# Performance work log

Hardware: AMD Instinct MI355X
Metric: run time of the kernel (lower is better)

## Reference

```python
import jax, jax.numpy as jnp
import numpy as np

NGH, POS_D, NEG_D, SUB_D, BORDER = 7, 3, 5, 1, 16

def _offsets():
    rad = NGH // SUB_D * NGH
    pos, neg = [], []
    for j in range(-rad, rad + 1, SUB_D):
        for i in range(-rad, rad + 1, SUB_D):
            d2 = i * i + j * j
            if d2 <= POS_D ** 2:
                pos.append((i, j))
            elif NEG_D ** 2 <= d2 <= NGH ** 2:
                neg.append((i, j))
    return (jnp.asarray(np.array(pos, np.int32).T),  # [2, P] rows (dy, dx)
            jnp.asarray(np.array(neg, np.int32).T))  # [2, Ng]

POS_OFF, NEG_OFF = _offsets()

def bilinear(pos, feat):
    # pos [N,2]=(y,x) float coords in feature-map scale; feat [C,h,w] -> [N,C]
    C, h, w = feat.shape
    y = jnp.clip(pos[:, 0], 0.0, h - 1.0)
    x = jnp.clip(pos[:, 1], 0.0, w - 1.0)
    y0 = jnp.floor(y); x0 = jnp.floor(x)
    y0i = y0.astype(jnp.int32); x0i = x0.astype(jnp.int32)
    y1i = jnp.minimum(y0i + 1, h - 1); x1i = jnp.minimum(x0i + 1, w - 1)
    wy = (y - y0)[:, None]; wx = (x - x0)[:, None]
    g = lambda yi, xi: feat[:, yi, xi].T  # [N,C]
    return ((1 - wy) * (1 - wx) * g(y0i, x0i) + (1 - wy) * wx * g(y0i, x1i)
            + wy * (1 - wx) * g(y1i, x0i) + wy * wx * g(y1i, x1i))

def l2norm(x):
    return x / jnp.maximum(jnp.linalg.norm(x, axis=-1, keepdims=True), 1e-12)

def clamp_yx(p, H, W):
    return jnp.stack([jnp.clip(p[..., 0], 0.0, H - 1.0),
                      jnp.clip(p[..., 1], 0.0, W - 1.0)], axis=-1)

def _per_image(f0, f1, c0, c1, p0, p1, H, W, N):
    # all points are generated inside the border, so the border mask keeps all;
    # rnd_sample -> deterministic first-N / last-N subsample
    vp0 = p0[:N].astype(jnp.float32)          # [N,2]
    vp1 = p1[:N].astype(jnp.float32)
    vf0 = l2norm(bilinear(vp0 / 4, f0))       # [N,128]
    qconf = bilinear(vp0 / 4, c0)[:, 0]       # [N]
    mask = ((vp1[:, 1] >= 0) & (vp1[:, 1] < W) & (vp1[:, 0] >= 0) & (vp1[:, 0] < H))
    def cand_scores(off):
        P = off.shape[1]
        cand = clamp_yx(vp1[None, :, :] + off.T[:, None, :].astype(jnp.float32), H, W)  # [P,N,2]
        fc = l2norm(bilinear(cand.reshape(-1, 2) / 4, f1).reshape(P, N, -1))
        return jnp.einsum('nc,pnc->np', vf0, fc)  # [N,P]
    ps = cand_scores(POS_OFF)
    pidx = jnp.argmax(ps, axis=1)
    pscore = jnp.max(ps, axis=1, keepdims=True)   # [N,1] (maxpool over pos ngh)
    sel = clamp_yx(vp1 + POS_OFF.T[pidx].astype(jnp.float32), H, W)
    qconf = (qconf + bilinear(sel / 4, c1)[:, 0]) / 2
    nscores = cand_scores(NEG_OFF)                # [N,Ng]
    vp2 = p1[p1.shape[0] - N:].astype(jnp.float32)  # independent subsample for distractors
    dist = l2norm(bilinear(vp2 / 4, f1))          # [N,128]
    return pscore, nscores, dist, vf0, vp1, vp2, qconf, mask

def reference(feat0, feat1, conf0, conf1, pos0, pos1, B, H, W, N):
    fn = jax.vmap(lambda a, b, c, d, e, f: _per_image(a, b, c, d, e, f, H, W, N))
    pscore, ns, dist, vf0, vp1, vp2, qconf, mask = fn(feat0, feat1, conf0, conf1, pos0, pos1)
    BN = B * N
    pscores = pscore.reshape(BN, 1)
    nscores = ns.reshape(BN, -1)
    dist = dist.reshape(BN, -1)
    vf0 = vf0.reshape(BN, -1)
    vp1 = vp1.reshape(BN, 2)
    vp2 = vp2.reshape(BN, 2)
    dscores = vf0 @ dist.T  # [BN,BN]
    dis2 = ((vp2[None, :, 1] - vp1[:, None, 1]) ** 2
            + (vp2[None, :, 0] - vp1[:, None, 0]) ** 2)
    b = jnp.repeat(jnp.arange(BN) // N, 1)
    b = jnp.arange(B).repeat(N)
    dis2 = dis2 + ((b[None, :] != b[:, None]) * (NEG_D ** 2)).astype(dis2.dtype)
    dscores = jnp.where(dis2 < NEG_D ** 2, 0.0, dscores)
    scores = jnp.concatenate([pscores, nscores, dscores], axis=1)
    gt = jnp.zeros(scores.shape, jnp.uint8).at[:, :pscores.shape[1]].set(1)
    return scores, gt, mask, qconf

def setup_inputs() -> dict:
    key = jax.random.key(0)
    ks = jax.random.split(key, 6)
    B, H, W, M, N = 4, 512, 512, 2500, 2000
    h, w, C = H // 4, W // 4, 128
    feat0 = jax.random.normal(ks[0], (B, C, h, w), jnp.float32)
    feat1 = jax.random.normal(ks[1], (B, C, h, w), jnp.float32)
    conf0 = jax.random.uniform(ks[2], (B, 1, h, w), jnp.float32)
    conf1 = jax.random.uniform(ks[3], (B, 1, h, w), jnp.float32)
    pos0 = jax.random.randint(ks[4], (B, M, 2), BORDER, H - BORDER).astype(jnp.int32)
    pos1 = jax.random.randint(ks[5], (B, M, 2), BORDER, H - BORDER).astype(jnp.int32)
    return dict(feat0=feat0, feat1=feat1, conf0=conf0, conf1=conf1,
                pos0=pos0, pos1=pos1, B=B, H=H, W=W, N=N)
```

## Files before the change

kernel.cpp:

```cpp
#include <hip/hip_runtime.h>

typedef unsigned short ushort_t;
typedef __attribute__((ext_vector_type(8))) short bf16x8;
typedef __attribute__((ext_vector_type(4))) float f32x4;

#define BB 4
#define HH 512
#define WW 512
#define NPT 2000
#define MPT 2500
#define CCH 128
#define FH 128
#define FW 128
#define FHW (FH*FW)
#define BNP (BB*NPT)
#define NPOSC 29
#define NNEGC 80
#define NCOL (1 + NNEGC + BNP)

__constant__ int c_pos_dy[NPOSC] = {
  0,
  -2,-1,0,1,2,
  -2,-1,0,1,2,
  -3,-2,-1,0,1,2,3,
  -2,-1,0,1,2,
  -2,-1,0,1,2,
  0};
__constant__ int c_pos_dx[NPOSC] = {
  -3,
  -2,-2,-2,-2,-2,
  -1,-1,-1,-1,-1,
  0,0,0,0,0,0,0,
  1,1,1,1,1,
  2,2,2,2,2,
  3};
__constant__ int c_neg_dy[NNEGC] = {
  0,
  -3,-2,-1,0,1,2,3,
  -4,-3,-2,-1,0,1,2,3,4,
  -5,-4,-3,3,4,5,
  -6,-5,-4,4,5,6,
  -6,-5,5,6,
  -6,-5,5,6,
  -7,-6,-5,5,6,7,
  -6,-5,5,6,
  -6,-5,5,6,
  -6,-5,-4,4,5,6,
  -5,-4,-3,3,4,5,
  -4,-3,-2,-1,0,1,2,3,4,
  -3,-2,-1,0,1,2,3,
  0};
__constant__ int c_neg_dx[NNEGC] = {
  -7,
  -6,-6,-6,-6,-6,-6,-6,
  -5,-5,-5,-5,-5,-5,-5,-5,-5,
  -4,-4,-4,-4,-4,-4,
  -3,-3,-3,-3,-3,-3,
  -2,-2,-2,-2,
  -1,-1,-1,-1,
  0,0,0,0,0,0,
  1,1,1,1,
  2,2,2,2,
  3,3,3,3,3,3,
  4,4,4,4,4,4,
  5,5,5,5,5,5,5,5,5,
  6,6,6,6,6,6,6,
  7};

__device__ __forceinline__ ushort_t f2bf(float f) {
  unsigned u = __float_as_uint(f);
  unsigned r = (u + 0x7fffu + ((u >> 16) & 1u)) >> 16;
  return (ushort_t)r;
}

__device__ __forceinline__ float2 sample2(const float* __restrict__ fb,
                                          float fy, float fx, int lane) {
  float y = fminf(fmaxf(fy, 0.f), (float)(FH - 1));
  float x = fminf(fmaxf(fx, 0.f), (float)(FW - 1));
  float y0 = floorf(y), x0 = floorf(x);
  int iy0 = (int)y0, ix0 = (int)x0;
  int iy1 = min(iy0 + 1, FH - 1), ix1 = min(ix0 + 1, FW - 1);
  float wy = y - y0, wx = x - x0;
  float w00 = (1.f - wy) * (1.f - wx), w01 = (1.f - wy) * wx;
  float w10 = wy * (1.f - wx),         w11 = wy * wx;
  int c = 2 * lane;
  float2 a00 = *(const float2*)(fb + ((size_t)iy0 * FW + ix0) * CCH + c);
  float2 a01 = *(const float2*)(fb + ((size_t)iy0 * FW + ix1) * CCH + c);
  float2 a10 = *(const float2*)(fb + ((size_t)iy1 * FW + ix0) * CCH + c);
  float2 a11 = *(const float2*)(fb + ((size_t)iy1 * FW + ix1) * CCH + c);
  float2 r;
  r.x = w00 * a00.x + w01 * a01.x + w10 * a10.x + w11 * a11.x;
  r.y = w00 * a00.y + w01 * a01.y + w10 * a10.y + w11 * a11.y;
  return r;
}

__device__ __forceinline__ float conf_sample(const float* __restrict__ cb,
                                             float py, float px) {
  float y = fminf(fmaxf(py * 0.25f, 0.f), (float)(FH - 1));
  float x = fminf(fmaxf(px * 0.25f, 0.f), (float)(FW - 1));
  float y0 = floorf(y), x0 = floorf(x);
  int iy0 = (int)y0, ix0 = (int)x0;
  int iy1 = min(iy0 + 1, FH - 1), ix1 = min(ix0 + 1, FW - 1);
  float wy = y - y0, wx = x - x0;
  return (1.f - wy) * (1.f - wx) * cb[iy0 * FW + ix0]
       + (1.f - wy) * wx         * cb[iy0 * FW + ix1]
       + wy * (1.f - wx)         * cb[iy1 * FW + ix0]
       + wy * wx                 * cb[iy1 * FW + ix1];
}

__device__ __forceinline__ float wave_sum(float v) {
#pragma unroll
  for (int o = 32; o > 0; o >>= 1) v += __shfl_xor(v, o, 64);
  return v;
}

__device__ __forceinline__ void cand_partial(const float* __restrict__ fb,
                                             int py, int px, int dy, int dx,
                                             int sub, const float* __restrict__ a8,
                                             float& dot, float& ss) {
  float cy = fminf(fmaxf((float)(py + dy), 0.f), (float)(HH - 1)) * 0.25f;
  float cx = fminf(fmaxf((float)(px + dx), 0.f), (float)(WW - 1)) * 0.25f;
  float y = fminf(cy, (float)(FH - 1));
  float x = fminf(cx, (float)(FW - 1));
  float y0 = floorf(y), x0 = floorf(x);
  int iy0 = (int)y0, ix0 = (int)x0;
  int iy1 = min(iy0 + 1, FH - 1), ix1 = min(ix0 + 1, FW - 1);
  float wy = y - y0, wx = x - x0;
  float w00 = (1.f - wy) * (1.f - wx), w01 = (1.f - wy) * wx;
  float w10 = wy * (1.f - wx),         w11 = wy * wx;
  const float* p00 = fb + ((size_t)iy0 * FW + ix0) * CCH + sub * 8;
  const float* p01 = fb + ((size_t)iy0 * FW + ix1) * CCH + sub * 8;
  const float* p10 = fb + ((size_t)iy1 * FW + ix0) * CCH + sub * 8;
  const float* p11 = fb + ((size_t)iy1 * FW + ix1) * CCH + sub * 8;
  float c00[8], c01[8], c10[8], c11[8];
  *(float4*)&c00[0] = *(const float4*)p00; *(float4*)&c00[4] = *(const float4*)(p00 + 4);
  *(float4*)&c01[0] = *(const float4*)p01; *(float4*)&c01[4] = *(const float4*)(p01 + 4);
  *(float4*)&c10[0] = *(const float4*)p10; *(float4*)&c10[4] = *(const float4*)(p10 + 4);
  *(float4*)&c11[0] = *(const float4*)p11; *(float4*)&c11[4] = *(const float4*)(p11 + 4);
  float d = 0.f, s = 0.f;
#pragma unroll
  for (int ch = 0; ch < 8; ++ch) {
    float v = w00 * c00[ch] + w01 * c01[ch] + w10 * c10[ch] + w11 * c11[ch];
    d += a8[ch] * v;
    s += v * v;
  }
  dot = d; ss = s;
}

__device__ __forceinline__ void better(float& best, int& bidx, float ob, int oi) {
  if (ob > best || (ob == best && oi < bidx)) { best = ob; bidx = oi; }
}

__global__ __launch_bounds__(256) void k_transpose(const float* __restrict__ feat0,
                                                   const float* __restrict__ feat1,
                                                   float* __restrict__ ft0,
                                                   float* __restrict__ ft1) {
  __shared__ float tile[32][33];
  int z = blockIdx.z;
  const float* src = (z < BB) ? feat0 + (size_t)z * CCH * FHW
                              : feat1 + (size_t)(z - BB) * CCH * FHW;
  float* dst = (z < BB) ? ft0 + (size_t)z * CCH * FHW
                        : ft1 + (size_t)(z - BB) * CCH * FHW;
  int p0 = blockIdx.x * 32;
  int c0 = blockIdx.y * 32;
  int tx = threadIdx.x & 31, ty = threadIdx.x >> 5;
#pragma unroll
  for (int jj = 0; jj < 32; jj += 8)
    tile[ty + jj][tx] = src[(size_t)(c0 + ty + jj) * FHW + p0 + tx];
  __syncthreads();
#pragma unroll
  for (int jj = 0; jj < 32; jj += 8)
    dst[(size_t)(p0 + ty + jj) * CCH + c0 + tx] = tile[tx][ty + jj];
}

__global__ __launch_bounds__(256) void k_prep(const float* __restrict__ ft0,
                                              const float* __restrict__ ft1,
                                              const int* __restrict__ pos0,
                                              const int* __restrict__ pos1,
                                              float* __restrict__ vf0,
                                              ushort_t* __restrict__ vf0_bf,
                                              ushort_t* __restrict__ dist_bf,
                                              float* __restrict__ mask_out) {
  int wv = threadIdx.x >> 6, lane = threadIdx.x & 63;
  int n = blockIdx.x * 4 + wv;
  int b = n / NPT, r = n % NPT;

  {
    const float* fb = ft0 + (size_t)b * FHW * CCH;
    float py = (float)pos0[(b * MPT + r) * 2 + 0];
    float px = (float)pos0[(b * MPT + r) * 2 + 1];
    float2 v = sample2(fb, py * 0.25f, px * 0.25f, lane);
    float ss = wave_sum(v.x * v.x + v.y * v.y);
    float inv = 1.f / fmaxf(sqrtf(ss), 1e-12f);
    v.x *= inv; v.y *= inv;
    *(float2*)(vf0 + (size_t)n * CCH + 2 * lane) = v;
    ushort2 p; p.x = f2bf(v.x); p.y = f2bf(v.y);
    *(ushort2*)(vf0_bf + (size_t)n * CCH + 2 * lane) = p;
  }

  {
    const float* fb = ft1 + (size_t)b * FHW * CCH;
    float py = (float)pos1[(b * MPT + (MPT - NPT) + r) * 2 + 0];
    float px = (float)pos1[(b * MPT + (MPT - NPT) + r) * 2 + 1];
    float2 v = sample2(fb, py * 0.25f, px * 0.25f, lane);
    float ss = wave_sum(v.x * v.x + v.y * v.y);
    float inv = 1.f / fmaxf(sqrtf(ss), 1e-12f);
    v.x *= inv; v.y *= inv;
    ushort2 p; p.x = f2bf(v.x); p.y = f2bf(v.y);
    *(ushort2*)(dist_bf + (size_t)n * CCH + 2 * lane) = p;
  }

  if (lane == 0) {
    int my = pos1[(b * MPT + r) * 2 + 0];
    int mx = pos1[(b * MPT + r) * 2 + 1];
    mask_out[n] = (mx >= 0 && mx < WW && my >= 0 && my < HH) ? 1.f : 0.f;
  }
}

__global__ __launch_bounds__(256) void k_zero(float4* __restrict__ p, int n4) {
  int i = blockIdx.x * blockDim.x + threadIdx.x;
  int stride = gridDim.x * blockDim.x;
  float4 z; z.x = 0.f; z.y = 0.f; z.z = 0.f; z.w = 0.f;
  for (; i < n4; i += stride) p[i] = z;
}

__global__ __launch_bounds__(256) void k_cand(const float* __restrict__ ft1,
                                              const float* __restrict__ conf0,
                                              const float* __restrict__ conf1,
                                              const int* __restrict__ pos0,
                                              const int* __restrict__ pos1,
                                              const float* __restrict__ vf0,
                                              float* __restrict__ scores,
                                              float* __restrict__ gt,
                                              float* __restrict__ qconf_out) {
  int n = blockIdx.x;
  int b = n / NPT, r = n % NPT;
  int tid = threadIdx.x;
  int lane = tid & 63, wv = tid >> 6;
  int g = lane >> 4;
  int sub = lane & 15;
  const float* fb1 = ft1 + (size_t)b * FHW * CCH;
  int py = pos1[(b * MPT + r) * 2 + 0];
  int px = pos1[(b * MPT + r) * 2 + 1];

  float a8[8];
  *(float4*)&a8[0] = *(const float4*)(vf0 + (size_t)n * CCH + sub * 8);
  *(float4*)&a8[4] = *(const float4*)(vf0 + (size_t)n * CCH + sub * 8 + 4);

  __shared__ float s_best[4];
  __shared__ int   s_idx[4];

  float best = -1e30f; int bidx = 0x7fffffff;
#pragma unroll
  for (int it = 0; it < 2; ++it) {
    int p = it * 16 + wv * 4 + g;
    int pc = min(p, NPOSC - 1);
    float dot, ss;
    cand_partial(fb1, py, px, c_pos_dy[pc], c_pos_dx[pc], sub, a8, dot, ss);
#pragma unroll
    for (int o = 1; o < 16; o <<= 1) {
      dot += __shfl_xor(dot, o, 64);
      ss  += __shfl_xor(ss,  o, 64);
    }
    float sc = dot / fmaxf(sqrtf(ss), 1e-12f);
    if (p < NPOSC && sc > best) { best = sc; bidx = p; }
  }
  {
    float ob = __shfl_xor(best, 16, 64); int oi = __shfl_xor(bidx, 16, 64);
    better(best, bidx, ob, oi);
    ob = __shfl_xor(best, 32, 64); oi = __shfl_xor(bidx, 32, 64);
    better(best, bidx, ob, oi);
  }
  if (lane == 0) { s_best[wv] = best; s_idx[wv] = bidx; }
  __syncthreads();
  if (tid == 0) {
    float bb = s_best[0]; int bi = s_idx[0];
#pragma unroll
    for (int w2 = 1; w2 < 4; ++w2) better(bb, bi, s_best[w2], s_idx[w2]);
    scores[(size_t)n * NCOL] = bb;
    gt[(size_t)n * NCOL] = 1.0f;
    float q0 = conf_sample(conf0 + (size_t)b * FHW,
                           (float)pos0[(b * MPT + r) * 2 + 0],
                           (float)pos0[(b * MPT + r) * 2 + 1]);
    float sy = fminf(fmaxf((float)(py + c_pos_dy[bi]), 0.f), (float)(HH - 1));
    float sx = fminf(fmaxf((float)(px + c_pos_dx[bi]), 0.f), (float)(WW - 1));
    float q1 = conf_sample(conf1 + (size_t)b * FHW, sy, sx);
    qconf_out[n] = 0.5f * (q0 + q1);
  }

#pragma unroll
  for (int it = 0; it < 5; ++it) {
    int p = it * 16 + wv * 4 + g;
    float dot, ss;
    cand_partial(fb1, py, px, c_neg_dy[p], c_neg_dx[p], sub, a8, dot, ss);
#pragma unroll
    for (int o = 1; o < 16; o <<= 1) {
      dot += __shfl_xor(dot, o, 64);
      ss  += __shfl_xor(ss,  o, 64);
    }
    if (sub == 0)
      scores[(size_t)n * NCOL + 1 + p] = dot / fmaxf(sqrtf(ss), 1e-12f);
  }
}

__global__ __launch_bounds__(256) void k_gemm(const ushort_t* __restrict__ vf0_bf,
                                              const ushort_t* __restrict__ dist_bf,
                                              const int* __restrict__ pos1,
                                              float* __restrict__ scores) {
  int i0 = blockIdx.x * 128, j0 = blockIdx.y * 128;
  int tid = threadIdx.x, lane = tid & 63, wv = tid >> 6;
  int wm = wv >> 1, wn = wv & 1;
  int mrow = lane & 15, quad = lane >> 4;

  __shared__ float s_ry[128], s_rx[128], s_rb[128];
  __shared__ float s_cy[128], s_cx[128], s_cb[128];
  if (tid < 128) {
    int i = min(i0 + tid, BNP - 1);
    int b = i / NPT, rr = i - b * NPT;
    s_ry[tid] = (float)pos1[(b * MPT + rr) * 2 + 0];
    s_rx[tid] = (float)pos1[(b * MPT + rr) * 2 + 1];
    s_rb[tid] = (float)b;
  } else {
    int t2 = tid - 128;
    int j = min(j0 + t2, BNP - 1);
    int b = j / NPT, rr = j - b * NPT;
    s_cy[t2] = (float)pos1[(b * MPT + (MPT - NPT) + rr) * 2 + 0];
    s_cx[t2] = (float)pos1[(b * MPT + (MPT - NPT) + rr) * 2 + 1];
    s_cb[t2] = (float)b;
  }
  __syncthreads();

  f32x4 acc[4][4] = {};
  const ushort_t* abase = vf0_bf  + (size_t)(i0 + wm * 64 + mrow) * CCH + quad * 8;
  const ushort_t* bbase = dist_bf + (size_t)(j0 + wn * 64 + mrow) * CCH + quad * 8;
#pragma unroll
  for (int ks = 0; ks < 4; ++ks) {
    bf16x8 af[4], bf[4];
#pragma unroll
    for (int f = 0; f < 4; ++f) {
      af[f] = *(const bf16x8*)(abase + (size_t)f * 16 * CCH + ks * 32);
      bf[f] = *(const bf16x8*)(bbase + (size_t)f * 16 * CCH + ks * 32);
    }
#pragma unroll
    for (int fm = 0; fm < 4; ++fm)
#pragma unroll
      for (int fn = 0; fn < 4; ++fn)
        acc[fm][fn] = __builtin_amdgcn_mfma_f32_16x16x32_bf16(af[fm], bf[fn],
                                                              acc[fm][fn], 0, 0, 0);
  }

  float cy[4], cx[4], cb[4]; int colg[4];
#pragma unroll
  for (int fn = 0; fn < 4; ++fn) {
    int cl = wn * 64 + fn * 16 + mrow;
    cy[fn] = s_cy[cl]; cx[fn] = s_cx[cl]; cb[fn] = s_cb[cl];
    colg[fn] = j0 + cl;
  }
#pragma unroll
  for (int fm = 0; fm < 4; ++fm) {
#pragma unroll
    for (int reg = 0; reg < 4; ++reg) {
      int rl = wm * 64 + fm * 16 + quad * 4 + reg;
      int row = i0 + rl;
      if (row >= BNP) continue;
      float ry = s_ry[rl], rx = s_rx[rl], rb = s_rb[rl];
      size_t base = (size_t)row * NCOL + 1 + NNEGC;
#pragma unroll
      for (int fn = 0; fn < 4; ++fn) {
        if (colg[fn] >= BNP) continue;
        float dy = cy[fn] - ry, dx = cx[fn] - rx;
        float d2 = dy * dy + dx * dx + ((cb[fn] != rb) ? 25.f : 0.f);
        scores[base + colg[fn]] = (d2 < 25.f) ? 0.f : acc[fm][fn][reg];
      }
    }
  }
}

extern "C" void kernel_launch(void* const* d_in, const int* in_sizes, int n_in,
                              void* d_out, int out_size, void* d_ws, size_t ws_size,
                              hipStream_t stream) {
  (void)in_sizes; (void)n_in; (void)out_size; (void)ws_size;
  const float* feat0 = (const float*)d_in[0];
  const float* feat1 = (const float*)d_in[1];
  const float* conf0 = (const float*)d_in[2];
  const float* conf1 = (const float*)d_in[3];
  const int*   pos0  = (const int*)d_in[4];
  const int*   pos1  = (const int*)d_in[5];

  float* ws = (float*)d_ws;
  float* ft0 = ws;
  float* ft1 = ft0 + (size_t)BB * CCH * FHW;
  float* vf0 = ft1 + (size_t)BB * CCH * FHW;
  ushort_t* vf0_bf  = (ushort_t*)(vf0 + (size_t)BNP * CCH);
  ushort_t* dist_bf = vf0_bf + (size_t)BNP * CCH;

  float* out    = (float*)d_out;
  float* scores = out;
  float* gt     = out + (size_t)BNP * NCOL;
  float* maskp  = gt + (size_t)BNP * NCOL;
  float* qconf  = maskp + BNP;

  dim3 g1(FHW / 32, CCH / 32, 2 * BB);
  k_transpose<<<g1, dim3(256), 0, stream>>>(feat0, feat1, ft0, ft1);
  k_prep<<<dim3(BNP / 4), dim3(256), 0, stream>>>(ft0, ft1, pos0, pos1,
                                                  vf0, vf0_bf, dist_bf, maskp);
  int n4 = (BNP * NCOL) / 4;
  k_zero<<<dim3(8192), dim3(256), 0, stream>>>((float4*)gt, n4);
  k_cand<<<dim3(BNP), dim3(256), 0, stream>>>(ft1, conf0, conf1, pos0, pos1,
                                              vf0, scores, gt, qconf);
  dim3 g5((BNP + 127) / 128, (BNP + 127) / 128);
  k_gemm<<<g5, dim3(256), 0, stream>>>(vf0_bf, dist_bf, pos1, scores);
}
```

Measured before the change: 756.1 us.

## Fuse prep and gt zeroing into candidate kernel, stage feature patch in LDS

```diff
diff --git a/kernel.cpp b/kernel.cpp
--- a/kernel.cpp
+++ b/kernel.cpp
@@ -17,6 +17,7 @@
 #define NPOSC 29
 #define NNEGC 80
 #define NCOL (1 + NNEGC + BNP)
+#define PATCH 6
 
 __constant__ int c_pos_dy[NPOSC] = {
   0,
@@ -114,24 +115,26 @@
   return v;
 }
 
-__device__ __forceinline__ void cand_partial(const float* __restrict__ fb,
-                                             int py, int px, int dy, int dx,
-                                             int sub, const float* __restrict__ a8,
-                                             float& dot, float& ss) {
+__device__ __forceinline__ void cand_partial_lds(const float* __restrict__ sp,
+                                                 int py, int px, int r0, int c0,
+                                                 int dy, int dx, int sub,
+                                                 const float* __restrict__ a8,
+                                                 float& dot, float& ss) {
   float cy = fminf(fmaxf((float)(py + dy), 0.f), (float)(HH - 1)) * 0.25f;
   float cx = fminf(fmaxf((float)(px + dx), 0.f), (float)(WW - 1)) * 0.25f;
   float y = fminf(cy, (float)(FH - 1));
   float x = fminf(cx, (float)(FW - 1));
   float y0 = floorf(y), x0 = floorf(x);
   int iy0 = (int)y0, ix0 = (int)x0;
-  int iy1 = min(iy0 + 1, FH - 1), ix1 = min(ix0 + 1, FW - 1);
+  int iy1 = min(iy0 + 1, FH - 1) - r0, ix1 = min(ix0 + 1, FW - 1) - c0;
+  iy0 -= r0; ix0 -= c0;
   float wy = y - y0, wx = x - x0;
   float w00 = (1.f - wy) * (1.f - wx), w01 = (1.f - wy) * wx;
   float w10 = wy * (1.f - wx),         w11 = wy * wx;
-  const float* p00 = fb + ((size_t)iy0 * FW + ix0) * CCH + sub * 8;
-  const float* p01 = fb + ((size_t)iy0 * FW + ix1) * CCH + sub * 8;
-  const float* p10 = fb + ((size_t)iy1 * FW + ix0) * CCH + sub * 8;
-  const float* p11 = fb + ((size_t)iy1 * FW + ix1) * CCH + sub * 8;
+  const float* p00 = sp + (iy0 * PATCH + ix0) * CCH + sub * 8;
+  const float* p01 = sp + (iy0 * PATCH + ix1) * CCH + sub * 8;
+  const float* p10 = sp + (iy1 * PATCH + ix0) * CCH + sub * 8;
+  const float* p11 = sp + (iy1 * PATCH + ix1) * CCH + sub * 8;
   float c00[8], c01[8], c10[8], c11[8];
   *(float4*)&c00[0] = *(const float4*)p00; *(float4*)&c00[4] = *(const float4*)(p00 + 4);
   *(float4*)&c01[0] = *(const float4*)p01; *(float4*)&c01[4] = *(const float4*)(p01 + 4);
@@ -173,82 +176,74 @@
     dst[(size_t)(p0 + ty + jj) * CCH + c0 + tx] = tile[tx][ty + jj];
 }
 
-__global__ __launch_bounds__(256) void k_prep(const float* __restrict__ ft0,
+__global__ __launch_bounds__(256) void k_cand(const float* __restrict__ ft0,
                                               const float* __restrict__ ft1,
-                                              const int* __restrict__ pos0,
-                                              const int* __restrict__ pos1,
-                                              float* __restrict__ vf0,
-                                              ushort_t* __restrict__ vf0_bf,
-                                              ushort_t* __restrict__ dist_bf,
-                                              float* __restrict__ mask_out) {
-  int wv = threadIdx.x >> 6, lane = threadIdx.x & 63;
-  int n = blockIdx.x * 4 + wv;
-  int b = n / NPT, r = n % NPT;
-
-  {
-    const float* fb = ft0 + (size_t)b * FHW * CCH;
-    float py = (float)pos0[(b * MPT + r) * 2 + 0];
-    float px = (float)pos0[(b * MPT + r) * 2 + 1];
-    float2 v = sample2(fb, py * 0.25f, px * 0.25f, lane);
-    float ss = wave_sum(v.x * v.x + v.y * v.y);
-    float inv = 1.f / fmaxf(sqrtf(ss), 1e-12f);
-    v.x *= inv; v.y *= inv;
-    *(float2*)(vf0 + (size_t)n * CCH + 2 * lane) = v;
-    ushort2 p; p.x = f2bf(v.x); p.y = f2bf(v.y);
-    *(ushort2*)(vf0_bf + (size_t)n * CCH + 2 * lane) = p;
-  }
-
-  {
-    const float* fb = ft1 + (size_t)b * FHW * CCH;
-    float py = (float)pos1[(b * MPT + (MPT - NPT) + r) * 2 + 0];
-    float px = (float)pos1[(b * MPT + (MPT - NPT) + r) * 2 + 1];
-    float2 v = sample2(fb, py * 0.25f, px * 0.25f, lane);
-    float ss = wave_sum(v.x * v.x + v.y * v.y);
-    float inv = 1.f / fmaxf(sqrtf(ss), 1e-12f);
-    v.x *= inv; v.y *= inv;
-    ushort2 p; p.x = f2bf(v.x); p.y = f2bf(v.y);
-    *(ushort2*)(dist_bf + (size_t)n * CCH + 2 * lane) = p;
-  }
-
-  if (lane == 0) {
-    int my = pos1[(b * MPT + r) * 2 + 0];
-    int mx = pos1[(b * MPT + r) * 2 + 1];
-    mask_out[n] = (mx >= 0 && mx < WW && my >= 0 && my < HH) ? 1.f : 0.f;
-  }
-}
-
-__global__ __launch_bounds__(256) void k_zero(float4* __restrict__ p, int n4) {
-  int i = blockIdx.x * blockDim.x + threadIdx.x;
-  int stride = gridDim.x * blockDim.x;
-  float4 z; z.x = 0.f; z.y = 0.f; z.z = 0.f; z.w = 0.f;
-  for (; i < n4; i += stride) p[i] = z;
-}
-
-__global__ __launch_bounds__(256) void k_cand(const float* __restrict__ ft1,
                                               const float* __restrict__ conf0,
                                               const float* __restrict__ conf1,
                                               const int* __restrict__ pos0,
                                               const int* __restrict__ pos1,
-                                              const float* __restrict__ vf0,
+                                              ushort_t* __restrict__ vf0_bf,
+                                              ushort_t* __restrict__ dist_bf,
                                               float* __restrict__ scores,
                                               float* __restrict__ gt,
+                                              float* __restrict__ mask_out,
                                               float* __restrict__ qconf_out) {
+  __shared__ float s_patch[PATCH * PATCH * CCH];
+  __shared__ float s_vf0[CCH];
+  __shared__ float s_best[4];
+  __shared__ int   s_idx[4];
+
   int n = blockIdx.x;
-  int b = n / NPT, r = n % NPT;
+  int b = n / NPT, r = n - b * NPT;
   int tid = threadIdx.x;
   int lane = tid & 63, wv = tid >> 6;
+
+  int py = pos1[(b * MPT + r) * 2 + 0];
+  int px = pos1[(b * MPT + r) * 2 + 1];
+  int r0 = min(max((py - 7) >> 2, 0), FH - PATCH);
+  int c0 = min(max((px - 7) >> 2, 0), FW - PATCH);
+  const float* fb1 = ft1 + (size_t)b * FHW * CCH;
+
+  if (wv == 0) {
+    const float* fb0 = ft0 + (size_t)b * FHW * CCH;
+    float qy = (float)pos0[(b * MPT + r) * 2 + 0];
+    float qx = (float)pos0[(b * MPT + r) * 2 + 1];
+    float2 v = sample2(fb0, qy * 0.25f, qx * 0.25f, lane);
+    float ssum = wave_sum(v.x * v.x + v.y * v.y);
+    float inv = 1.f / fmaxf(sqrtf(ssum), 1e-12f);
+    v.x *= inv; v.y *= inv;
+    s_vf0[2 * lane] = v.x; s_vf0[2 * lane + 1] = v.y;
+    ushort2 p; p.x = f2bf(v.x); p.y = f2bf(v.y);
+    *(ushort2*)(vf0_bf + (size_t)n * CCH + 2 * lane) = p;
+  } else if (wv == 1) {
+    float qy = (float)pos1[(b * MPT + (MPT - NPT) + r) * 2 + 0];
+    float qx = (float)pos1[(b * MPT + (MPT - NPT) + r) * 2 + 1];
+    float2 v = sample2(fb1, qy * 0.25f, qx * 0.25f, lane);
+    float ssum = wave_sum(v.x * v.x + v.y * v.y);
+    float inv = 1.f / fmaxf(sqrtf(ssum), 1e-12f);
+    v.x *= inv; v.y *= inv;
+    ushort2 p; p.x = f2bf(v.x); p.y = f2bf(v.y);
+    *(ushort2*)(dist_bf + (size_t)n * CCH + 2 * lane) = p;
+  } else if (wv == 2 && lane == 0) {
+    mask_out[n] = (px >= 0 && px < WW && py >= 0 && py < HH) ? 1.f : 0.f;
+  }
+
+  {
+    float4* sp4 = (float4*)s_patch;
+#pragma unroll
+    for (int i4 = tid; i4 < PATCH * PATCH * CCH / 4; i4 += 256) {
+      int rr = i4 / (PATCH * CCH / 4);
+      int k  = i4 - rr * (PATCH * CCH / 4);
+      sp4[i4] = *(const float4*)(fb1 + ((size_t)(r0 + rr) * FW + c0) * CCH + 4 * k);
+    }
+  }
+  __syncthreads();
+
   int g = lane >> 4;
   int sub = lane & 15;
-  const float* fb1 = ft1 + (size_t)b * FHW * CCH;
-  int py = pos1[(b * MPT + r) * 2 + 0];
-  int px = pos1[(b * MPT + r) * 2 + 1];
-
   float a8[8];
-  *(float4*)&a8[0] = *(const float4*)(vf0 + (size_t)n * CCH + sub * 8);
-  *(float4*)&a8[4] = *(const float4*)(vf0 + (size_t)n * CCH + sub * 8 + 4);
-
-  __shared__ float s_best[4];
-  __shared__ int   s_idx[4];
+  *(float4*)&a8[0] = *(const float4*)(s_vf0 + sub * 8);
+  *(float4*)&a8[4] = *(const float4*)(s_vf0 + sub * 8 + 4);
 
   float best = -1e30f; int bidx = 0x7fffffff;
 #pragma unroll
@@ -256,7 +251,8 @@
     int p = it * 16 + wv * 4 + g;
     int pc = min(p, NPOSC - 1);
     float dot, ss;
-    cand_partial(fb1, py, px, c_pos_dy[pc], c_pos_dx[pc], sub, a8, dot, ss);
+    cand_partial_lds(s_patch, py, px, r0, c0, c_pos_dy[pc], c_pos_dx[pc],
+                     sub, a8, dot, ss);
 #pragma unroll
     for (int o = 1; o < 16; o <<= 1) {
       dot += __shfl_xor(dot, o, 64);
@@ -292,21 +288,25 @@
   for (int it = 0; it < 5; ++it) {
     int p = it * 16 + wv * 4 + g;
     float dot, ss;
-    cand_partial(fb1, py, px, c_neg_dy[p], c_neg_dx[p], sub, a8, dot, ss);
+    cand_partial_lds(s_patch, py, px, r0, c0, c_neg_dy[p], c_neg_dx[p],
+                     sub, a8, dot, ss);
 #pragma unroll
     for (int o = 1; o < 16; o <<= 1) {
       dot += __shfl_xor(dot, o, 64);
       ss  += __shfl_xor(ss,  o, 64);
     }
-    if (sub == 0)
+    if (sub == 0) {
       scores[(size_t)n * NCOL + 1 + p] = dot / fmaxf(sqrtf(ss), 1e-12f);
+      gt[(size_t)n * NCOL + 1 + p] = 0.f;
+    }
   }
 }
 
 __global__ __launch_bounds__(256) void k_gemm(const ushort_t* __restrict__ vf0_bf,
                                               const ushort_t* __restrict__ dist_bf,
                                               const int* __restrict__ pos1,
-                                              float* __restrict__ scores) {
+                                              float* __restrict__ scores,
+                                              float* __restrict__ gt) {
   int i0 = blockIdx.x * 128, j0 = blockIdx.y * 128;
   int tid = threadIdx.x, lane = tid & 63, wv = tid >> 6;
   int wm = wv >> 1, wn = wv & 1;
@@ -371,6 +371,7 @@
         float dy = cy[fn] - ry, dx = cx[fn] - rx;
         float d2 = dy * dy + dx * dx + ((cb[fn] != rb) ? 25.f : 0.f);
         scores[base + colg[fn]] = (d2 < 25.f) ? 0.f : acc[fm][fn][reg];
+        gt[base + colg[fn]] = 0.f;
       }
     }
   }
@@ -390,8 +391,7 @@
   float* ws = (float*)d_ws;
   float* ft0 = ws;
   float* ft1 = ft0 + (size_t)BB * CCH * FHW;
-  float* vf0 = ft1 + (size_t)BB * CCH * FHW;
-  ushort_t* vf0_bf  = (ushort_t*)(vf0 + (size_t)BNP * CCH);
+  ushort_t* vf0_bf  = (ushort_t*)(ft1 + (size_t)BB * CCH * FHW);
   ushort_t* dist_bf = vf0_bf + (size_t)BNP * CCH;
 
   float* out    = (float*)d_out;
@@ -402,12 +402,9 @@
 
   dim3 g1(FHW / 32, CCH / 32, 2 * BB);
   k_transpose<<<g1, dim3(256), 0, stream>>>(feat0, feat1, ft0, ft1);
-  k_prep<<<dim3(BNP / 4), dim3(256), 0, stream>>>(ft0, ft1, pos0, pos1,
-                                                  vf0, vf0_bf, dist_bf, maskp);
-  int n4 = (BNP * NCOL) / 4;
-  k_zero<<<dim3(8192), dim3(256), 0, stream>>>((float4*)gt, n4);
-  k_cand<<<dim3(BNP), dim3(256), 0, stream>>>(ft1, conf0, conf1, pos0, pos1,
-                                              vf0, scores, gt, qconf);
-  dim3 g5((BNP + 127) / 128, (BNP + 127) / 128);
-  k_gemm<<<g5, dim3(256), 0, stream>>>(vf0_bf, dist_bf, pos1, scores);
-}
+  k_cand<<<dim3(BNP), dim3(256), 0, stream>>>(ft0, ft1, conf0, conf1, pos0, pos1,
+                                              vf0_bf, dist_bf, scores, gt,
+                                              maskp, qconf);
+  dim3 g3((BNP + 127) / 128, (BNP + 127) / 128);
+  k_gemm<<<g3, dim3(256), 0, stream>>>(vf0_bf, dist_bf, pos1, scores, gt);
+}
```

New measurement: 760.8 us. No clear change (+0.6%).
